# Optimization experiments

Hardware: AMD Instinct MI355X
Metric: run time of the kernel (lower is better)

The kernel has to match this reference:

```python
import jax, jax.numpy as jnp
import numpy as np

INPUT_DIM, PROJ_DIM, HIDDEN = 1, 16, 32
B, T = 2048, 2048


def setup_inputs() -> dict:
    key = jax.random.key(0)
    ks = jax.random.split(key, 9)
    s_in = 1.0 / np.sqrt(INPUT_DIM)
    s_h = 1.0 / np.sqrt(HIDDEN)
    s_p = 1.0 / np.sqrt(PROJ_DIM)
    return {
        "x_seq": jax.random.normal(ks[0], (B, T, INPUT_DIM), dtype=jnp.float32),
        # input_linear: Linear(input_dim, proj_dim)
        "Wp": jax.random.uniform(ks[1], (PROJ_DIM, INPUT_DIM), minval=-s_in, maxval=s_in),
        "bp": jax.random.uniform(ks[2], (PROJ_DIM,), minval=-s_in, maxval=s_in),
        # LSTM weights (PyTorch gate order i,f,g,o)
        "W_ih": jax.random.uniform(ks[3], (4 * HIDDEN, PROJ_DIM), minval=-s_h, maxval=s_h),
        "W_hh": jax.random.uniform(ks[4], (4 * HIDDEN, HIDDEN), minval=-s_h, maxval=s_h),
        "b_ih": jax.random.uniform(ks[5], (4 * HIDDEN,), minval=-s_h, maxval=s_h),
        "b_hh": jax.random.uniform(ks[6], (4 * HIDDEN,), minval=-s_h, maxval=s_h),
        # output_linear: Linear(hidden, input_dim)
        "Wo": jax.random.uniform(ks[7], (INPUT_DIM, HIDDEN), minval=-s_h, maxval=s_h),
        "bo": jax.random.uniform(ks[8], (INPUT_DIM,), minval=-s_h, maxval=s_h),
    }


def reference(x_seq, Wp, bp, W_ih, W_hh, b_ih, b_hh, Wo, bo):
    H = W_hh.shape[1]
    b, t, _ = x_seq.shape
    # input projection for all timesteps at once (same math as per-step Linear)
    # then pre-apply W_ih: [B,T,4H]
    xp = jnp.einsum("bti,pi->btp", x_seq, Wp) + bp
    gates_x = jnp.einsum("btp,gp->btg", xp, W_ih) + b_ih + b_hh
    gates_x = jnp.transpose(gates_x, (1, 0, 2))  # [T,B,4H]

    def step(carry, gx):
        h, c = carry
        gates = gx + h @ W_hh.T  # [B,4H]
        i, f, g, o = jnp.split(gates, 4, axis=-1)
        i = jax.nn.sigmoid(i)
        f = jax.nn.sigmoid(f)
        g = jnp.tanh(g)
        o = jax.nn.sigmoid(o)
        c = f * c + i * g
        h = o * jnp.tanh(c)
        return (h, c), h

    h0 = jnp.zeros((b, H), dtype=x_seq.dtype)
    c0 = jnp.zeros((b, H), dtype=x_seq.dtype)
    (_, _), hs = jax.lax.scan(step, (h0, c0), gates_x)  # hs: [T,B,H]
    outputs = jnp.einsum("tbh,oh->bto", hs, Wo) + bo  # [B,T,input_dim]
    return outputs
```

## Files before the change

### kernel.cpp

```cpp
#include <hip/hip_runtime.h>


#define BB 2048
#define TT 2048
#define HH 32

typedef _Float16 h2 __attribute__((ext_vector_type(2)));

__device__ __forceinline__ float gate_eval(float x, float m, float a, float b) {
    float e = __builtin_amdgcn_exp2f(x * m);
    float r = __builtin_amdgcn_rcpf(1.0f + e);
    return fmaf(a, r, b);
}

template <int CTRL>
__device__ __forceinline__ float dpp_add(float v) {
    int s = __builtin_amdgcn_update_dpp(0, __float_as_int(v), CTRL, 0xf, 0xf, true);
    return v + __int_as_float(s);
}

struct HVec { h2 v[16]; };

__device__ __forceinline__ HVec gather_h(const _Float16* base) {
    const float4* p = (const float4*)base;
    float4 q0 = p[0], q1 = p[1], q2 = p[2], q3 = p[3];
    HVec r;
    r.v[0]  = __builtin_bit_cast(h2, q0.x); r.v[1]  = __builtin_bit_cast(h2, q0.y);
    r.v[2]  = __builtin_bit_cast(h2, q0.z); r.v[3]  = __builtin_bit_cast(h2, q0.w);
    r.v[4]  = __builtin_bit_cast(h2, q1.x); r.v[5]  = __builtin_bit_cast(h2, q1.y);
    r.v[6]  = __builtin_bit_cast(h2, q1.z); r.v[7]  = __builtin_bit_cast(h2, q1.w);
    r.v[8]  = __builtin_bit_cast(h2, q2.x); r.v[9]  = __builtin_bit_cast(h2, q2.y);
    r.v[10] = __builtin_bit_cast(h2, q2.z); r.v[11] = __builtin_bit_cast(h2, q2.w);
    r.v[12] = __builtin_bit_cast(h2, q3.x); r.v[13] = __builtin_bit_cast(h2, q3.y);
    r.v[14] = __builtin_bit_cast(h2, q3.z); r.v[15] = __builtin_bit_cast(h2, q3.w);
    return r;
}

__global__ __launch_bounds__(256) void lstm_fused_kernel(
    const float* __restrict__ x_seq,
    const float* __restrict__ Wp,
    const float* __restrict__ bp,
    const float* __restrict__ W_ih,
    const float* __restrict__ W_hh,
    const float* __restrict__ b_ih,
    const float* __restrict__ b_hh,
    const float* __restrict__ Wo,
    const float* __restrict__ bo,
    float* __restrict__ out)
{
    const int tid  = threadIdx.x;
    const int wave = tid >> 6;
    const int lane = tid & 63;
    const int half = lane >> 5;
    const int j    = lane & 31;
    const int b    = blockIdx.x * 8 + wave * 2 + half;

    const int rI = j, rF = HH + j, rG = 2 * HH + j, rO = 3 * HH + j;

    h2 wI[16], wF[16], wG[16], wO[16];
    {
        const float2* pI = (const float2*)(W_hh + rI * HH);
        const float2* pF = (const float2*)(W_hh + rF * HH);
        const float2* pG = (const float2*)(W_hh + rG * HH);
        const float2* pO = (const float2*)(W_hh + rO * HH);
#pragma unroll
        for (int k = 0; k < 16; ++k) {
            float2 a = pI[k], f = pF[k], g = pG[k], o = pO[k];
            wI[k].x = (_Float16)a.x; wI[k].y = (_Float16)a.y;
            wF[k].x = (_Float16)f.x; wF[k].y = (_Float16)f.y;
            wG[k].x = (_Float16)g.x; wG[k].y = (_Float16)g.y;
            wO[k].x = (_Float16)o.x; wO[k].y = (_Float16)o.y;
        }
    }

    float aI = 0.f, cI = 0.f, aF = 0.f, cF = 0.f;
    float aG = 0.f, cG = 0.f, aO = 0.f, cO = 0.f;
#pragma unroll
    for (int p = 0; p < 16; ++p) {
        float wpv = Wp[p], bpv = bp[p];
        float wi = W_ih[rI * 16 + p], wf = W_ih[rF * 16 + p];
        float wg = W_ih[rG * 16 + p], wo_ = W_ih[rO * 16 + p];
        aI = fmaf(wi, wpv, aI);  cI = fmaf(wi, bpv, cI);
        aF = fmaf(wf, wpv, aF);  cF = fmaf(wf, bpv, cF);
        aG = fmaf(wg, wpv, aG);  cG = fmaf(wg, bpv, cG);
        aO = fmaf(wo_, wpv, aO); cO = fmaf(wo_, bpv, cO);
    }
    cI += b_ih[rI] + b_hh[rI];
    cF += b_ih[rF] + b_hh[rF];
    cG += b_ih[rG] + b_hh[rG];
    cO += b_ih[rO] + b_hh[rO];

    const float LOG2E = 1.44269504088896340736f;
    const float woj = Wo[j];
    const float bo0 = bo[0];

    __shared__ __align__(16) _Float16 hsh[4][2][HH];
    _Float16* hbase = &hsh[wave][half][0];
    hbase[j] = (_Float16)0.0f;

    float c = 0.0f;
    const float* xp = x_seq + (size_t)b * TT;
    float* op = out + (size_t)b * TT;

    HVec hcur = gather_h(hbase);
    float4 x4 = *(const float4*)(xp);

    for (int t = 0; t < TT; t += 4) {
        const int tn = (t + 4 < TT) ? (t + 4) : t;
        float4 x4n = *(const float4*)(xp + tn);
        float outv[4];
#pragma unroll
        for (int u = 0; u < 4; ++u) {
            float xv = (u == 0) ? x4.x : (u == 1) ? x4.y : (u == 2) ? x4.z : x4.w;

            float sI0 = cI, sI1 = xv * aI;
            float sF0 = cF, sF1 = xv * aF;
            float sG0 = cG, sG1 = xv * aG;
            float sO0 = cO, sO1 = xv * aO;
#pragma unroll
            for (int k = 0; k < 16; k += 2) {
                h2 h0 = hcur.v[k], h1 = hcur.v[k + 1];
                sI0 = __builtin_amdgcn_fdot2(wI[k],     h0, sI0, false);
                sF0 = __builtin_amdgcn_fdot2(wF[k],     h0, sF0, false);
                sG0 = __builtin_amdgcn_fdot2(wG[k],     h0, sG0, false);
                sO0 = __builtin_amdgcn_fdot2(wO[k],     h0, sO0, false);
                sI1 = __builtin_amdgcn_fdot2(wI[k + 1], h1, sI1, false);
                sF1 = __builtin_amdgcn_fdot2(wF[k + 1], h1, sF1, false);
                sG1 = __builtin_amdgcn_fdot2(wG[k + 1], h1, sG1, false);
                sO1 = __builtin_amdgcn_fdot2(wO[k + 1], h1, sO1, false);
            }

            float iv = gate_eval(sI0 + sI1, -LOG2E, 1.0f, 0.0f);
            float fv = gate_eval(sF0 + sF1, -LOG2E, 1.0f, 0.0f);
            float gv = gate_eval(sG0 + sG1, -2.0f * LOG2E, 2.0f, -1.0f);
            float ov = gate_eval(sO0 + sO1, -LOG2E, 1.0f, 0.0f);

            c = fmaf(fv, c, iv * gv);
            float th = gate_eval(c, -2.0f * LOG2E, 2.0f, -1.0f);
            float h = ov * th;

            hbase[j] = (_Float16)h;
            hcur = gather_h(hbase);

            float po = woj * h;
            po = dpp_add<0x111>(po);
            po = dpp_add<0x112>(po);
            po = dpp_add<0x114>(po);
            po = dpp_add<0x118>(po);
            po = dpp_add<0x142>(po);
            outv[u] = po + bo0;
        }
        if ((lane & 31) == 31) {
            *(float4*)(op + t) = make_float4(outv[0], outv[1], outv[2], outv[3]);
        }
        x4 = x4n;
    }
}

extern "C" void kernel_launch(void* const* d_in, const int* in_sizes, int n_in,
                              void* d_out, int out_size, void* d_ws, size_t ws_size,
                              hipStream_t stream) {
    const float* x_seq = (const float*)d_in[0];
    const float* Wp    = (const float*)d_in[1];
    const float* bp    = (const float*)d_in[2];
    const float* W_ih  = (const float*)d_in[3];
    const float* W_hh  = (const float*)d_in[4];
    const float* b_ih  = (const float*)d_in[5];
    const float* b_hh  = (const float*)d_in[6];
    const float* Wo    = (const float*)d_in[7];
    const float* bo    = (const float*)d_in[8];
    float* out = (float*)d_out;

    dim3 grid(BB / 8);
    dim3 block(256);
    lstm_fused_kernel<<<grid, block, 0, stream>>>(
        x_seq, Wp, bp, W_ih, W_hh, b_ih, b_hh, Wo, bo, out);
}
```

Measured before the change: 672.4 us.

## Split LSTM gates across wave halves, one batch row per wave

Each wave now handles a single batch row instead of two. The two 32-lane halves each compute two of the four gate pre-activations (i/g on one half, f/o on the other) with half as many fdot2 operations and transcendental evaluations per lane. The activated gates are exchanged between halves with permlane32_swap, and the grid is doubled. This is meant to shorten the serial per-timestep latency chain and put two waves on each SIMD to hide latency. The cost is the extra cross-lane swaps and redundant cell-state and h computation in both halves.

```diff
diff --git a/kernel.cpp b/kernel.cpp
--- a/kernel.cpp
+++ b/kernel.cpp
@@ -6,6 +6,7 @@
 #define HH 32
 
 typedef _Float16 h2 __attribute__((ext_vector_type(2)));
+typedef unsigned int uint2v __attribute__((ext_vector_type(2)));
 
 __device__ __forceinline__ float gate_eval(float x, float m, float a, float b) {
     float e = __builtin_amdgcn_exp2f(x * m);
@@ -53,44 +54,39 @@
     const int lane = tid & 63;
     const int half = lane >> 5;
     const int j    = lane & 31;
-    const int b    = blockIdx.x * 8 + wave * 2 + half;
+    const int b    = blockIdx.x * 4 + wave;
 
-    const int rI = j, rF = HH + j, rG = 2 * HH + j, rO = 3 * HH + j;
+    const int rA = half * HH + j;
+    const int rB = 2 * HH + half * HH + j;
 
-    h2 wI[16], wF[16], wG[16], wO[16];
+    h2 wA[16], wB[16];
     {
-        const float2* pI = (const float2*)(W_hh + rI * HH);
-        const float2* pF = (const float2*)(W_hh + rF * HH);
-        const float2* pG = (const float2*)(W_hh + rG * HH);
-        const float2* pO = (const float2*)(W_hh + rO * HH);
+        const float2* pA = (const float2*)(W_hh + rA * HH);
+        const float2* pB = (const float2*)(W_hh + rB * HH);
 #pragma unroll
         for (int k = 0; k < 16; ++k) {
-            float2 a = pI[k], f = pF[k], g = pG[k], o = pO[k];
-            wI[k].x = (_Float16)a.x; wI[k].y = (_Float16)a.y;
-            wF[k].x = (_Float16)f.x; wF[k].y = (_Float16)f.y;
-            wG[k].x = (_Float16)g.x; wG[k].y = (_Float16)g.y;
-            wO[k].x = (_Float16)o.x; wO[k].y = (_Float16)o.y;
+            float2 a = pA[k], q = pB[k];
+            wA[k].x = (_Float16)a.x; wA[k].y = (_Float16)a.y;
+            wB[k].x = (_Float16)q.x; wB[k].y = (_Float16)q.y;
         }
     }
 
-    float aI = 0.f, cI = 0.f, aF = 0.f, cF = 0.f;
-    float aG = 0.f, cG = 0.f, aO = 0.f, cO = 0.f;
+    float xA = 0.f, kA = 0.f, xB = 0.f, kB = 0.f;
 #pragma unroll
     for (int p = 0; p < 16; ++p) {
         float wpv = Wp[p], bpv = bp[p];
-        float wi = W_ih[rI * 16 + p], wf = W_ih[rF * 16 + p];
-        float wg = W_ih[rG * 16 + p], wo_ = W_ih[rO * 16 + p];
-        aI = fmaf(wi, wpv, aI);  cI = fmaf(wi, bpv, cI);
-        aF = fmaf(wf, wpv, aF);  cF = fmaf(wf, bpv, cF);
-        aG = fmaf(wg, wpv, aG);  cG = fmaf(wg, bpv, cG);
-        aO = fmaf(wo_, wpv, aO); cO = fmaf(wo_, bpv, cO);
+        float wa = W_ih[rA * 16 + p], wb = W_ih[rB * 16 + p];
+        xA = fmaf(wa, wpv, xA);  kA = fmaf(wa, bpv, kA);
+        xB = fmaf(wb, wpv, xB);  kB = fmaf(wb, bpv, kB);
     }
-    cI += b_ih[rI] + b_hh[rI];
-    cF += b_ih[rF] + b_hh[rF];
-    cG += b_ih[rG] + b_hh[rG];
-    cO += b_ih[rO] + b_hh[rO];
+    kA += b_ih[rA] + b_hh[rA];
+    kB += b_ih[rB] + b_hh[rB];
 
     const float LOG2E = 1.44269504088896340736f;
+    const float mB = half ? -LOG2E : -2.0f * LOG2E;
+    const float aB = half ? 1.0f   : 2.0f;
+    const float bB = half ? 0.0f   : -1.0f;
+
     const float woj = Wo[j];
     const float bo0 = bo[0];
 
@@ -113,27 +109,28 @@
         for (int u = 0; u < 4; ++u) {
             float xv = (u == 0) ? x4.x : (u == 1) ? x4.y : (u == 2) ? x4.z : x4.w;
 
-            float sI0 = cI, sI1 = xv * aI;
-            float sF0 = cF, sF1 = xv * aF;
-            float sG0 = cG, sG1 = xv * aG;
-            float sO0 = cO, sO1 = xv * aO;
+            float sA0 = kA, sA1 = xv * xA;
+            float sB0 = kB, sB1 = xv * xB;
 #pragma unroll
             for (int k = 0; k < 16; k += 2) {
                 h2 h0 = hcur.v[k], h1 = hcur.v[k + 1];
-                sI0 = __builtin_amdgcn_fdot2(wI[k],     h0, sI0, false);
-                sF0 = __builtin_amdgcn_fdot2(wF[k],     h0, sF0, false);
-                sG0 = __builtin_amdgcn_fdot2(wG[k],     h0, sG0, false);
-                sO0 = __builtin_amdgcn_fdot2(wO[k],     h0, sO0, false);
-                sI1 = __builtin_amdgcn_fdot2(wI[k + 1], h1, sI1, false);
-                sF1 = __builtin_amdgcn_fdot2(wF[k + 1], h1, sF1, false);
-                sG1 = __builtin_amdgcn_fdot2(wG[k + 1], h1, sG1, false);
-                sO1 = __builtin_amdgcn_fdot2(wO[k + 1], h1, sO1, false);
+                sA0 = __builtin_amdgcn_fdot2(wA[k],     h0, sA0, false);
+                sB0 = __builtin_amdgcn_fdot2(wB[k],     h0, sB0, false);
+                sA1 = __builtin_amdgcn_fdot2(wA[k + 1], h1, sA1, false);
+                sB1 = __builtin_amdgcn_fdot2(wB[k + 1], h1, sB1, false);
             }
 
-            float iv = gate_eval(sI0 + sI1, -LOG2E, 1.0f, 0.0f);
-            float fv = gate_eval(sF0 + sF1, -LOG2E, 1.0f, 0.0f);
-            float gv = gate_eval(sG0 + sG1, -2.0f * LOG2E, 2.0f, -1.0f);
-            float ov = gate_eval(sO0 + sO1, -LOG2E, 1.0f, 0.0f);
+            float Aact = gate_eval(sA0 + sA1, -LOG2E, 1.0f, 0.0f);
+            float Bact = gate_eval(sB0 + sB1, mB, aB, bB);
+
+            uint2v eA = __builtin_amdgcn_permlane32_swap(
+                __float_as_uint(Aact), __float_as_uint(Aact), false, false);
+            uint2v eB = __builtin_amdgcn_permlane32_swap(
+                __float_as_uint(Bact), __float_as_uint(Bact), false, false);
+            float iv = __uint_as_float(eA[0]);
+            float fv = __uint_as_float(eA[1]);
+            float gv = __uint_as_float(eB[0]);
+            float ov = __uint_as_float(eB[1]);
 
             c = fmaf(fv, c, iv * gv);
             float th = gate_eval(c, -2.0f * LOG2E, 2.0f, -1.0f);
@@ -150,7 +147,7 @@
             po = dpp_add<0x142>(po);
             outv[u] = po + bo0;
         }
-        if ((lane & 31) == 31) {
+        if (lane == 31) {
             *(float4*)(op + t) = make_float4(outv[0], outv[1], outv[2], outv[3]);
         }
         x4 = x4n;
@@ -171,7 +168,7 @@
     const float* bo    = (const float*)d_in[8];
     float* out = (float*)d_out;
 
-    dim3 grid(BB / 8);
+    dim3 grid(BB / 4);
     dim3 block(256);
     lstm_fused_kernel<<<grid, block, 0, stream>>>(
         x_seq, Wp, bp, W_ih, W_hh, b_ih, b_hh, Wo, bo, out);
```

After: 783.2 us. 16.5% more time.

## Broadcast hidden state via DPP and permlane32 swaps instead of LDS

Applied to the files above, without the earlier changes.

Replaces the per-step LDS write and 64-byte readback of the hidden vector with a register-only all-gather built from DPP quad and row rotations plus permlane32_swap. The lane-to-hidden-unit mapping is rearranged so each batch row spans lanes from both 32-lane halves. The recurrent weights are loaded in a permuted order so they line up with the gathered packed-half2 layout. The output reduction likewise uses permlane32_swap in place of row_bcast. The aim is to take LDS latency and the wait on its write-read dependency off the serial time-step critical path, at the cost of more DPP/permlane instructions per step and fragile index bookkeeping.

```diff
diff --git a/kernel.cpp b/kernel.cpp
--- a/kernel.cpp
+++ b/kernel.cpp
@@ -6,6 +6,7 @@
 #define HH 32
 
 typedef _Float16 h2 __attribute__((ext_vector_type(2)));
+typedef unsigned int uint2v __attribute__((ext_vector_type(2)));
 
 __device__ __forceinline__ float gate_eval(float x, float m, float a, float b) {
     float e = __builtin_amdgcn_exp2f(x * m);
@@ -14,27 +15,20 @@
 }
 
 template <int CTRL>
+__device__ __forceinline__ int dpp_i(int v) {
+    return __builtin_amdgcn_update_dpp(0, v, CTRL, 0xf, 0xf, true);
+}
+
+template <int CTRL>
 __device__ __forceinline__ float dpp_add(float v) {
     int s = __builtin_amdgcn_update_dpp(0, __float_as_int(v), CTRL, 0xf, 0xf, true);
     return v + __int_as_float(s);
 }
 
-struct HVec { h2 v[16]; };
-
-__device__ __forceinline__ HVec gather_h(const _Float16* base) {
-    const float4* p = (const float4*)base;
-    float4 q0 = p[0], q1 = p[1], q2 = p[2], q3 = p[3];
-    HVec r;
-    r.v[0]  = __builtin_bit_cast(h2, q0.x); r.v[1]  = __builtin_bit_cast(h2, q0.y);
-    r.v[2]  = __builtin_bit_cast(h2, q0.z); r.v[3]  = __builtin_bit_cast(h2, q0.w);
-    r.v[4]  = __builtin_bit_cast(h2, q1.x); r.v[5]  = __builtin_bit_cast(h2, q1.y);
-    r.v[6]  = __builtin_bit_cast(h2, q1.z); r.v[7]  = __builtin_bit_cast(h2, q1.w);
-    r.v[8]  = __builtin_bit_cast(h2, q2.x); r.v[9]  = __builtin_bit_cast(h2, q2.y);
-    r.v[10] = __builtin_bit_cast(h2, q2.z); r.v[11] = __builtin_bit_cast(h2, q2.w);
-    r.v[12] = __builtin_bit_cast(h2, q3.x); r.v[13] = __builtin_bit_cast(h2, q3.y);
-    r.v[14] = __builtin_bit_cast(h2, q3.z); r.v[15] = __builtin_bit_cast(h2, q3.w);
-    return r;
-}
+#define DPP_XOR1 0xB1
+#define DPP_XOR2 0x4E
+#define DPP_ROR4 0x124
+#define DPP_ROR8 0x128
 
 __global__ __launch_bounds__(256) void lstm_fused_kernel(
     const float* __restrict__ x_seq,
@@ -51,25 +45,51 @@
     const int tid  = threadIdx.x;
     const int wave = tid >> 6;
     const int lane = tid & 63;
-    const int half = lane >> 5;
-    const int j    = lane & 31;
-    const int b    = blockIdx.x * 8 + wave * 2 + half;
+    const int brow = (lane >> 4) & 1;
+    const int j    = (lane & 15) | ((lane >> 5) << 4);
+    const int b    = blockIdx.x * 8 + wave * 2 + brow;
 
     const int rI = j, rF = HH + j, rG = 2 * HH + j, rO = 3 * HH + j;
 
-    h2 wI[16], wF[16], wG[16], wO[16];
+    int iL0 = j;
+    int iH0 = dpp_i<DPP_XOR1>(iL0);
+    int iL1 = dpp_i<DPP_XOR2>(iL0), iH1 = dpp_i<DPP_XOR2>(iH0);
+    int iL2 = dpp_i<DPP_ROR4>(iL0), iH2 = dpp_i<DPP_ROR4>(iH0);
+    int iL3 = dpp_i<DPP_ROR4>(iL1), iH3 = dpp_i<DPP_ROR4>(iH1);
+    int iL4 = dpp_i<DPP_ROR8>(iL0), iH4 = dpp_i<DPP_ROR8>(iH0);
+    int iL5 = dpp_i<DPP_ROR8>(iL1), iH5 = dpp_i<DPP_ROR8>(iH1);
+    int iL6 = dpp_i<DPP_ROR8>(iL2), iH6 = dpp_i<DPP_ROR8>(iH2);
+    int iL7 = dpp_i<DPP_ROR8>(iL3), iH7 = dpp_i<DPP_ROR8>(iH3);
+
+    int idx0L[8], idx1L[8], idx0H[8], idx1H[8];
     {
-        const float2* pI = (const float2*)(W_hh + rI * HH);
-        const float2* pF = (const float2*)(W_hh + rF * HH);
-        const float2* pG = (const float2*)(W_hh + rG * HH);
-        const float2* pO = (const float2*)(W_hh + rO * HH);
-#pragma unroll
-        for (int k = 0; k < 16; ++k) {
-            float2 a = pI[k], f = pF[k], g = pG[k], o = pO[k];
-            wI[k].x = (_Float16)a.x; wI[k].y = (_Float16)a.y;
-            wF[k].x = (_Float16)f.x; wF[k].y = (_Float16)f.y;
-            wG[k].x = (_Float16)g.x; wG[k].y = (_Float16)g.y;
-            wO[k].x = (_Float16)o.x; wO[k].y = (_Float16)o.y;
+        const int tL[8] = {iL0, iL1, iL2, iL3, iL4, iL5, iL6, iL7};
+        const int tH[8] = {iH0, iH1, iH2, iH3, iH4, iH5, iH6, iH7};
+#pragma unroll
+        for (int p = 0; p < 8; ++p) {
+            uint2v r = __builtin_amdgcn_permlane32_swap((unsigned)tL[p], (unsigned)tL[p], false, false);
+            idx0L[p] = (int)r[0]; idx1L[p] = (int)r[1];
+            uint2v q = __builtin_amdgcn_permlane32_swap((unsigned)tH[p], (unsigned)tH[p], false, false);
+            idx0H[p] = (int)q[0]; idx1H[p] = (int)q[1];
+        }
+    }
+
+    h2 wI0[8], wI1[8], wF0[8], wF1[8], wG0[8], wG1[8], wO0[8], wO1[8];
+    {
+        const float* WI = W_hh + rI * HH;
+        const float* WF = W_hh + rF * HH;
+        const float* WG = W_hh + rG * HH;
+        const float* WO = W_hh + rO * HH;
+#pragma unroll
+        for (int p = 0; p < 8; ++p) {
+            wI0[p].x = (_Float16)WI[idx0L[p]]; wI0[p].y = (_Float16)WI[idx0H[p]];
+            wI1[p].x = (_Float16)WI[idx1L[p]]; wI1[p].y = (_Float16)WI[idx1H[p]];
+            wF0[p].x = (_Float16)WF[idx0L[p]]; wF0[p].y = (_Float16)WF[idx0H[p]];
+            wF1[p].x = (_Float16)WF[idx1L[p]]; wF1[p].y = (_Float16)WF[idx1H[p]];
+            wG0[p].x = (_Float16)WG[idx0L[p]]; wG0[p].y = (_Float16)WG[idx0H[p]];
+            wG1[p].x = (_Float16)WG[idx1L[p]]; wG1[p].y = (_Float16)WG[idx1H[p]];
+            wO0[p].x = (_Float16)WO[idx0L[p]]; wO0[p].y = (_Float16)WO[idx0H[p]];
+            wO1[p].x = (_Float16)WO[idx1L[p]]; wO1[p].y = (_Float16)WO[idx1H[p]];
         }
     }
 
@@ -94,15 +114,14 @@
     const float woj = Wo[j];
     const float bo0 = bo[0];
 
-    __shared__ __align__(16) _Float16 hsh[4][2][HH];
-    _Float16* hbase = &hsh[wave][half][0];
-    hbase[j] = (_Float16)0.0f;
+    unsigned m0[8], m1[8];
+#pragma unroll
+    for (int p = 0; p < 8; ++p) { m0[p] = 0u; m1[p] = 0u; }
 
     float c = 0.0f;
     const float* xp = x_seq + (size_t)b * TT;
     float* op = out + (size_t)b * TT;
 
-    HVec hcur = gather_h(hbase);
     float4 x4 = *(const float4*)(xp);
 
     for (int t = 0; t < TT; t += 4) {
@@ -118,16 +137,17 @@
             float sG0 = cG, sG1 = xv * aG;
             float sO0 = cO, sO1 = xv * aO;
 #pragma unroll
-            for (int k = 0; k < 16; k += 2) {
-                h2 h0 = hcur.v[k], h1 = hcur.v[k + 1];
-                sI0 = __builtin_amdgcn_fdot2(wI[k],     h0, sI0, false);
-                sF0 = __builtin_amdgcn_fdot2(wF[k],     h0, sF0, false);
-                sG0 = __builtin_amdgcn_fdot2(wG[k],     h0, sG0, false);
-                sO0 = __builtin_amdgcn_fdot2(wO[k],     h0, sO0, false);
-                sI1 = __builtin_amdgcn_fdot2(wI[k + 1], h1, sI1, false);
-                sF1 = __builtin_amdgcn_fdot2(wF[k + 1], h1, sF1, false);
-                sG1 = __builtin_amdgcn_fdot2(wG[k + 1], h1, sG1, false);
-                sO1 = __builtin_amdgcn_fdot2(wO[k + 1], h1, sO1, false);
+            for (int p = 0; p < 8; ++p) {
+                h2 h0 = __builtin_bit_cast(h2, m0[p]);
+                h2 h1 = __builtin_bit_cast(h2, m1[p]);
+                sI0 = __builtin_amdgcn_fdot2(wI0[p], h0, sI0, false);
+                sF0 = __builtin_amdgcn_fdot2(wF0[p], h0, sF0, false);
+                sG0 = __builtin_amdgcn_fdot2(wG0[p], h0, sG0, false);
+                sO0 = __builtin_amdgcn_fdot2(wO0[p], h0, sO0, false);
+                sI1 = __builtin_amdgcn_fdot2(wI1[p], h1, sI1, false);
+                sF1 = __builtin_amdgcn_fdot2(wF1[p], h1, sF1, false);
+                sG1 = __builtin_amdgcn_fdot2(wG1[p], h1, sG1, false);
+                sO1 = __builtin_amdgcn_fdot2(wO1[p], h1, sO1, false);
             }
 
             float iv = gate_eval(sI0 + sI1, -LOG2E, 1.0f, 0.0f);
@@ -139,18 +159,38 @@
             float th = gate_eval(c, -2.0f * LOG2E, 2.0f, -1.0f);
             float h = ov * th;
 
-            hbase[j] = (_Float16)h;
-            hcur = gather_h(hbase);
+            unsigned own = (unsigned)__builtin_bit_cast(unsigned short, (_Float16)h);
+            int nb = dpp_i<DPP_XOR1>((int)own);
+            unsigned q0 = own | ((unsigned)nb << 16);
+            unsigned q1 = (unsigned)dpp_i<DPP_XOR2>((int)q0);
+            unsigned q2 = (unsigned)dpp_i<DPP_ROR4>((int)q0);
+            unsigned q3 = (unsigned)dpp_i<DPP_ROR4>((int)q1);
+            unsigned q4 = (unsigned)dpp_i<DPP_ROR8>((int)q0);
+            unsigned q5 = (unsigned)dpp_i<DPP_ROR8>((int)q1);
+            unsigned q6 = (unsigned)dpp_i<DPP_ROR8>((int)q2);
+            unsigned q7 = (unsigned)dpp_i<DPP_ROR8>((int)q3);
+            {
+                uint2v r;
+                r = __builtin_amdgcn_permlane32_swap(q0, q0, false, false); m0[0] = r[0]; m1[0] = r[1];
+                r = __builtin_amdgcn_permlane32_swap(q1, q1, false, false); m0[1] = r[0]; m1[1] = r[1];
+                r = __builtin_amdgcn_permlane32_swap(q2, q2, false, false); m0[2] = r[0]; m1[2] = r[1];
+                r = __builtin_amdgcn_permlane32_swap(q3, q3, false, false); m0[3] = r[0]; m1[3] = r[1];
+                r = __builtin_amdgcn_permlane32_swap(q4, q4, false, false); m0[4] = r[0]; m1[4] = r[1];
+                r = __builtin_amdgcn_permlane32_swap(q5, q5, false, false); m0[5] = r[0]; m1[5] = r[1];
+                r = __builtin_amdgcn_permlane32_swap(q6, q6, false, false); m0[6] = r[0]; m1[6] = r[1];
+                r = __builtin_amdgcn_permlane32_swap(q7, q7, false, false); m0[7] = r[0]; m1[7] = r[1];
+            }
 
             float po = woj * h;
             po = dpp_add<0x111>(po);
             po = dpp_add<0x112>(po);
             po = dpp_add<0x114>(po);
             po = dpp_add<0x118>(po);
-            po = dpp_add<0x142>(po);
-            outv[u] = po + bo0;
-        }
-        if ((lane & 31) == 31) {
+            uint2v rr = __builtin_amdgcn_permlane32_swap(
+                __float_as_uint(po), __float_as_uint(po), false, false);
+            outv[u] = __uint_as_float(rr[0]) + __uint_as_float(rr[1]) + bo0;
+        }
+        if (lane < 32 && (lane & 15) == 15) {
             *(float4*)(op + t) = make_float4(outv[0], outv[1], outv[2], outv[3]);
         }
         x4 = x4n;
```

Result: slower. 734.0 us (+9.2%).
